# Performance work log

Hardware: AMD Instinct MI355X
Metric: run time of the kernel (lower is better)

## Reference

```python
import jax, jax.numpy as jnp
import numpy as np

K = 3          # conv kernel size
G = 3          # KAN grid intervals
SPLINE_K = 3   # B-spline order
N_BASIS = G + SPLINE_K  # 6


def extended_grid():
    # pykan-style grid on [-1, 1] with G intervals, extended by k knots each side
    h = 2.0 / G
    return jnp.arange(-SPLINE_K, G + SPLINE_K + 1, dtype=jnp.float32) * h - 1.0  # [G+2k+1]


def bspline_basis(x, t, k):
    """Cox-de Boor recursion. x: [...], t: [m] knots -> [..., m-1-k] bases."""
    x = x[..., None]
    b = ((x >= t[:-1]) & (x < t[1:])).astype(x.dtype)  # degree 0: [..., m-1]
    for d in range(1, k + 1):
        left = (x - t[: -(d + 1)]) / (t[d:-1] - t[: -(d + 1)]) * b[..., :-1]
        right = (t[d + 1:] - x) / (t[d + 1:] - t[1:-d]) * b[..., 1:]
        b = left + right
    return b  # [..., m-1-k]


def setup_inputs() -> dict:
    key = jax.random.key(0)
    k1, k2, k3, k4 = jax.random.split(key, 4)
    B, C, H, W = 32, 16, 64, 64
    in_dim, out_dim = C * K * K, 64
    x = jax.random.normal(k1, (B, C, H, W), dtype=jnp.float32)
    coef = jax.random.normal(k2, (in_dim, out_dim, N_BASIS), dtype=jnp.float32) * 0.1
    scale_base = jax.random.normal(k3, (in_dim, out_dim), dtype=jnp.float32) * (1.0 / np.sqrt(in_dim))
    scale_sp = jnp.ones((in_dim, out_dim), dtype=jnp.float32) + 0.0 * jax.random.normal(k4, (in_dim, out_dim))
    return {"x": x, "coef": coef, "scale_base": scale_base, "scale_sp": scale_sp}


def reference(x, coef, scale_base, scale_sp):
    B, C, H, W = x.shape
    Ho, Wo = H - K + 1, W - K + 1
    # im2col with torch-reshape ordering: feature index = c*K*K + di*K + dj
    cols = [x[:, :, di:di + Ho, dj:dj + Wo] for di in range(K) for dj in range(K)]
    patches = jnp.stack(cols, axis=2)                    # [B, C, K*K, Ho, Wo]
    patches = patches.reshape(B, C * K * K, Ho, Wo)      # [B, D, Ho, Wo]
    p = patches.transpose(0, 2, 3, 1)                    # [B, Ho, Wo, D]

    t = extended_grid()
    basis = bspline_basis(p, t, SPLINE_K)                # [B, Ho, Wo, D, N_BASIS]
    # spline part: sum over input dims and bases, with per-edge scale_sp folded into coef
    spline = jnp.einsum('bhwdn,don->bhwo', basis, coef * scale_sp[:, :, None])
    base = jnp.einsum('bhwd,do->bhwo', jax.nn.silu(p), scale_base)
    y = base + spline                                    # [B, Ho, Wo, O]
    return y.transpose(0, 3, 1, 2)                       # [B, O, Ho, Wo]
```

## Files before the change

kernel.cpp:

```cpp
#include <hip/hip_runtime.h>
#include <math.h>

#define Bsz 32
#define Cc  16
#define Hh  64
#define Ww  64
#define HO  62
#define WO  62
#define OD  64
#define ND  144
#define NCHUNK 36
#define BSKEW 520
#define BSM_U16 77824

using short8 = __attribute__((ext_vector_type(8))) short;
using f32x4  = __attribute__((ext_vector_type(4))) float;

__device__ __forceinline__ unsigned short f2bf(float f) {
    union { float f; unsigned u; } v; v.f = f;
    unsigned r = v.u + 0x7fff + ((v.u >> 16) & 1);
    return (unsigned short)(r >> 16);
}
__device__ __forceinline__ float bf2f(unsigned short h) {
    union { unsigned u; float f; } v; v.u = ((unsigned)h) << 16; return v.f;
}

__device__ __forceinline__ uint4 feat_pack(float xv) {
    float xi = (xv + 3.0f) * 1.5f;
    float fi = floorf(xi);
    int   ii = (int)fi;
    float u  = xi - fi;
    float u2 = u * u, u3 = u2 * u;
    float P0 = u3 * (1.0f / 6.0f);
    float P1 = (1.0f + 3.0f * u + 3.0f * u2 - 3.0f * u3) * (1.0f / 6.0f);
    float P2 = (4.0f - 6.0f * u2 + 3.0f * u3) * (1.0f / 6.0f);
    float om = 1.0f - u;
    float P3 = om * om * om * (1.0f / 6.0f);
    bool ok = (ii >= 0) && (ii <= 8);
    float bas[6];
    #pragma unroll
    for (int n = 0; n < 6; ++n) {
        int t = ii - n;
        float v = (t == 0) ? P0 : (t == 1) ? P1 : (t == 2) ? P2 : (t == 3) ? P3 : 0.0f;
        bas[n] = ok ? v : 0.0f;
    }
    float s = xv / (1.0f + __expf(-xv));
    unsigned short sh = f2bf(s);
    unsigned short sl = f2bf(s - bf2f(sh));
    uint4 pk;
    pk.x = (unsigned)f2bf(bas[0]) | ((unsigned)f2bf(bas[1]) << 16);
    pk.y = (unsigned)f2bf(bas[2]) | ((unsigned)f2bf(bas[3]) << 16);
    pk.z = (unsigned)f2bf(bas[4]) | ((unsigned)f2bf(bas[5]) << 16);
    pk.w = (unsigned)sh | ((unsigned)sl << 16);
    return pk;
}

__global__ __launch_bounds__(256) void kan_feat(const float* __restrict__ x,
                                                uint4* __restrict__ fg) {
    int base = blockIdx.x * 2048 + threadIdx.x;
    #pragma unroll
    for (int j = 0; j < 8; ++j) {
        int i = base + j * 256;
        fg[i] = feat_pack(x[i]);
    }
}

__global__ __launch_bounds__(256) void kan_prep2(const float* __restrict__ coef,
                                                 const float* __restrict__ sbase,
                                                 const float* __restrict__ ssp,
                                                 unsigned short* __restrict__ wps) {
    int p = blockIdx.x * 256 + threadIdx.x;
    if (p >= BSM_U16) return;
    int dd  = p / BSKEW;
    int rem = p - dd * BSKEW;
    int o = rem >> 3, n = rem & 7;
    float v = 0.0f;
    if (dd < ND && rem < 512)
        v = (n < 6) ? coef[(dd * OD + o) * 6 + n] * ssp[dd * OD + o] : sbase[dd * OD + o];
    wps[p] = f2bf(v);
}

__global__ __launch_bounds__(512) void kan_gemm(const uint4* __restrict__ fg,
                                                const unsigned short* __restrict__ wps,
                                                float* __restrict__ out) {
    __shared__ unsigned short bsm[BSM_U16];

    const int tid  = threadIdx.x;
    const int bb   = blockIdx.x >> 3;
    const int h    = (blockIdx.x & 7) * 8 + (tid >> 6);
    const int wid  = tid >> 6;
    const int lane = tid & 63;
    const int l15  = lane & 15;
    const int ks   = lane >> 4;
    const bool alive = (h < HO);

    {
        const uint4* src = (const uint4*)wps;
        uint4* dst = (uint4*)bsm;
        #pragma unroll
        for (int it = 0; it < 19; ++it) dst[it * 512 + tid] = src[it * 512 + tid];
    }
    __syncthreads();

    f32x4 acc[4][4];
    #pragma unroll
    for (int rt = 0; rt < 4; ++rt)
        #pragma unroll
        for (int ct = 0; ct < 4; ++ct) acc[rt][ct] = (f32x4){0.f, 0.f, 0.f, 0.f};

    if (alive) {
        const unsigned short* bbase = bsm + ks * BSKEW + l15 * 8;

        auto loadA = [&](int cb, short8* A) {
            int dd  = cb * 4 + ks;
            int c   = (dd * 57) >> 9;
            int rem = dd - c * 9;
            int di  = (rem * 11) >> 5;
            int dj  = rem - di * 3;
            const short8* ap = (const short8*)fg + ((((bb * Cc + c) << 6) + h + di) << 6) + l15 + dj;
            A[0] = ap[0]; A[1] = ap[16]; A[2] = ap[32]; A[3] = ap[48];
        };
        auto loadB = [&](int cb, short8* Bf) {
            const short8* bp = (const short8*)(bbase + cb * 4 * BSKEW);
            Bf[0] = bp[0]; Bf[1] = bp[16]; Bf[2] = bp[32]; Bf[3] = bp[48];
        };

        short8 A0[4], B0[4], A1[4], B1[4];
        loadA(0, A0); loadB(0, B0);
        for (int cb = 0; cb < NCHUNK; cb += 2) {
            loadA(cb + 1, A1); loadB(cb + 1, B1);
            #pragma unroll
            for (int rt = 0; rt < 4; ++rt)
                #pragma unroll
                for (int ct = 0; ct < 4; ++ct)
                    acc[rt][ct] = __builtin_amdgcn_mfma_f32_16x16x32_bf16(A0[rt], B0[ct], acc[rt][ct], 0, 0, 0);
            if (cb + 2 < NCHUNK) { loadA(cb + 2, A0); loadB(cb + 2, B0); }
            #pragma unroll
            for (int rt = 0; rt < 4; ++rt)
                #pragma unroll
                for (int ct = 0; ct < 4; ++ct)
                    acc[rt][ct] = __builtin_amdgcn_mfma_f32_16x16x32_bf16(A1[rt], B1[ct], acc[rt][ct], 0, 0, 0);
        }
    }

    __syncthreads();
    if (alive) {
        float* sc = (float*)bsm + wid * (OD * 68);
        #pragma unroll
        for (int rt = 0; rt < 4; ++rt)
            #pragma unroll
            for (int ct = 0; ct < 4; ++ct)
                *(f32x4*)&sc[(ct * 16 + l15) * 68 + rt * 16 + ks * 4] = acc[rt][ct];
        #pragma unroll 4
        for (int j = 0; j < OD; ++j) {
            float v = sc[j * 68 + lane];
            if (lane < WO) out[((bb * OD + j) * HO + h) * WO + lane] = v;
        }
    }
}

#define FW 68
__global__ __launch_bounds__(256) void kan_prep(const float* __restrict__ coef,
                                                const float* __restrict__ sbase,
                                                const float* __restrict__ ssp,
                                                unsigned short* __restrict__ wp) {
    int idx = blockIdx.x * 256 + threadIdx.x;
    if (idx >= ND * OD * 8) return;
    int n = idx & 7, o = (idx >> 3) & 63, d = idx >> 9;
    float v = (n < 6) ? coef[(d * OD + o) * 6 + n] * ssp[d * OD + o] : sbase[d * OD + o];
    wp[idx] = f2bf(v);
}

__global__ __launch_bounds__(128) void kan_mfma(const float* __restrict__ x,
                                                const unsigned short* __restrict__ wp,
                                                float* __restrict__ out) {
    __shared__ uint4 feat[Cc * 4 * FW];
    const int rp = blockIdx.x, b = blockIdx.y, tid = threadIdx.x;
    const int wid = tid >> 6, lane = tid & 63, l15 = lane & 15, ks = lane >> 4;
    const int hrow0 = rp * 2;
    for (int i = tid; i < Cc * 4 * FW; i += 128) {
        int wl = i % FW, cr = i / FW, r = cr & 3, c = cr >> 2;
        int col = wl < Ww ? wl : Ww - 1;
        feat[i] = feat_pack(x[((b * Cc + c) * Hh + hrow0 + r) * Ww + col]);
    }
    __syncthreads();
    f32x4 acc[4][4];
    #pragma unroll
    for (int rt = 0; rt < 4; ++rt)
        #pragma unroll
        for (int ct = 0; ct < 4; ++ct) acc[rt][ct] = (f32x4){0.f, 0.f, 0.f, 0.f};
    auto loadA = [&](int chunk, short8* A) {
        int d = chunk * 4 + ks;
        int c = (d * 57) >> 9;
        int rem = d - c * 9;
        int di = (rem * 11) >> 5;
        int dj = rem - di * 3;
        const short8* ap = (const short8*)&feat[(c * 4 + wid + di) * FW + l15 + dj];
        A[0] = ap[0]; A[1] = ap[16]; A[2] = ap[32]; A[3] = ap[48];
    };
    auto loadB = [&](int chunk, short8* Bf) {
        int d = chunk * 4 + ks;
        const short8* bp = (const short8*)wp + (d * 64 + l15);
        Bf[0] = bp[0]; Bf[1] = bp[16]; Bf[2] = bp[32]; Bf[3] = bp[48];
    };
    short8 A0[4], B0[4], A1[4], B1[4];
    loadA(0, A0); loadB(0, B0);
    for (int cb = 0; cb < NCHUNK; cb += 2) {
        loadA(cb + 1, A1); loadB(cb + 1, B1);
        #pragma unroll
        for (int rt = 0; rt < 4; ++rt)
            #pragma unroll
            for (int ct = 0; ct < 4; ++ct)
                acc[rt][ct] = __builtin_amdgcn_mfma_f32_16x16x32_bf16(A0[rt], B0[ct], acc[rt][ct], 0, 0, 0);
        if (cb + 2 < NCHUNK) { loadA(cb + 2, A0); loadB(cb + 2, B0); }
        #pragma unroll
        for (int rt = 0; rt < 4; ++rt)
            #pragma unroll
            for (int ct = 0; ct < 4; ++ct)
                acc[rt][ct] = __builtin_amdgcn_mfma_f32_16x16x32_bf16(A1[rt], B1[ct], acc[rt][ct], 0, 0, 0);
    }
    __syncthreads();
    float* sC = ((float*)feat) + wid * (OD * FW);
    #pragma unroll
    for (int rt = 0; rt < 4; ++rt)
        #pragma unroll
        for (int ct = 0; ct < 4; ++ct)
            *(f32x4*)&sC[(ct * 16 + l15) * FW + rt * 16 + ks * 4] = acc[rt][ct];
    const int orow = hrow0 + wid;
    for (int j = 0; j < OD; ++j) {
        float v = sC[j * FW + lane];
        if (lane < WO) out[((b * OD + j) * HO + orow) * WO + lane] = v;
    }
}

extern "C" void kernel_launch(void* const* d_in, const int* in_sizes, int n_in,
                              void* d_out, int out_size, void* d_ws, size_t ws_size,
                              hipStream_t stream) {
    (void)in_sizes; (void)n_in; (void)out_size;
    const float* x     = (const float*)d_in[0];
    const float* coef  = (const float*)d_in[1];
    const float* sbase = (const float*)d_in[2];
    const float* ssp   = (const float*)d_in[3];
    float* out = (float*)d_out;

    const size_t wps_bytes  = (size_t)BSM_U16 * 2;
    const size_t featg_bytes = (size_t)Bsz * Cc * Hh * Ww * 16;
    const size_t need = wps_bytes + featg_bytes + 64;

    if (ws_size >= need) {
        unsigned short* wps = (unsigned short*)d_ws;
        uint4* fg = (uint4*)((char*)d_ws + wps_bytes);
        kan_feat<<<1024, 256, 0, stream>>>(x, fg);
        kan_prep2<<<(BSM_U16 + 255) / 256, 256, 0, stream>>>(coef, sbase, ssp, wps);
        kan_gemm<<<256, 512, 0, stream>>>(fg, wps, out);
    } else if (ws_size >= (size_t)ND * OD * 8 * 2) {
        unsigned short* wp = (unsigned short*)d_ws;
        kan_prep<<<(ND * OD * 8 + 255) / 256, 256, 0, stream>>>(coef, sbase, ssp, wp);
        dim3 grid(HO / 2, Bsz);
        kan_mfma<<<grid, 128, 0, stream>>>(x, wp, out);
    }
}
```

Before: 48.29 us.

## Restructure KAN GEMM with 32x32 MFMA, LDS double-buffered async loads

Replaces the previous GEMM kernel with one where each 256-thread block computes two output rows for one batch. It stages both the feature tile and a K-chunk of weights into double-buffered LDS using global_load_lds, then runs 32x32x16 bf16 MFMAs. The weights are no longer kept whole in LDS, which cuts LDS use and allows more blocks per CU. The grid becomes 31x32 blocks instead of 256. The silu pair is packed so the duplicated base weight multiplies the hi and lo silu parts. The cost is a __syncthreads per K-chunk and smaller per-block reuse.

```diff
diff --git a/kernel.cpp b/kernel.cpp
--- a/kernel.cpp
+++ b/kernel.cpp
@@ -9,20 +9,27 @@
 #define WO  62
 #define OD  64
 #define ND  144
-#define NCHUNK 36
-#define BSKEW 520
-#define BSM_U16 77824
+#define KC  18
 
 using short8 = __attribute__((ext_vector_type(8))) short;
 using f32x4  = __attribute__((ext_vector_type(4))) float;
-
-__device__ __forceinline__ unsigned short f2bf(float f) {
+using f32x16 = __attribute__((ext_vector_type(16))) float;
+typedef unsigned int u32;
+typedef unsigned short ushort;
+
+__device__ __forceinline__ ushort f2bf(float f) {
     union { float f; unsigned u; } v; v.f = f;
     unsigned r = v.u + 0x7fff + ((v.u >> 16) & 1);
-    return (unsigned short)(r >> 16);
-}
-__device__ __forceinline__ float bf2f(unsigned short h) {
+    return (ushort)(r >> 16);
+}
+__device__ __forceinline__ float bf2f(ushort h) {
     union { unsigned u; float f; } v; v.u = ((unsigned)h) << 16; return v.f;
+}
+
+__device__ __forceinline__ void gload_lds16(const void* g, void* l) {
+    __builtin_amdgcn_global_load_lds((const __attribute__((address_space(1))) u32*)g,
+                                     (__attribute__((address_space(3))) u32*)l,
+                                     16, 0, 0);
 }
 
 __device__ __forceinline__ uint4 feat_pack(float xv) {
@@ -45,8 +52,8 @@
         bas[n] = ok ? v : 0.0f;
     }
     float s = xv / (1.0f + __expf(-xv));
-    unsigned short sh = f2bf(s);
-    unsigned short sl = f2bf(s - bf2f(sh));
+    ushort sh = f2bf(s);
+    ushort sl = f2bf(s - bf2f(sh));
     uint4 pk;
     pk.x = (unsigned)f2bf(bas[0]) | ((unsigned)f2bf(bas[1]) << 16);
     pk.y = (unsigned)f2bf(bas[2]) | ((unsigned)f2bf(bas[3]) << 16);
@@ -65,105 +72,121 @@
     }
 }
 
-__global__ __launch_bounds__(256) void kan_prep2(const float* __restrict__ coef,
+__global__ __launch_bounds__(256) void kan_prep3(const float* __restrict__ coef,
                                                  const float* __restrict__ sbase,
                                                  const float* __restrict__ ssp,
-                                                 unsigned short* __restrict__ wps) {
-    int p = blockIdx.x * 256 + threadIdx.x;
-    if (p >= BSM_U16) return;
-    int dd  = p / BSKEW;
-    int rem = p - dd * BSKEW;
-    int o = rem >> 3, n = rem & 7;
-    float v = 0.0f;
-    if (dd < ND && rem < 512)
-        v = (n < 6) ? coef[(dd * OD + o) * 6 + n] * ssp[dd * OD + o] : sbase[dd * OD + o];
-    wps[p] = f2bf(v);
-}
-
-__global__ __launch_bounds__(512) void kan_gemm(const uint4* __restrict__ fg,
-                                                const unsigned short* __restrict__ wps,
-                                                float* __restrict__ out) {
-    __shared__ unsigned short bsm[BSM_U16];
+                                                 ushort* __restrict__ wpb) {
+    int g = blockIdx.x * 256 + threadIdx.x;
+    if (g >= KC * 8 * 64) return;
+    int n = g & 63, d = g >> 6;
+    float sspv = ssp[d * OD + n];
+    ushort sb = f2bf(sbase[d * OD + n]);
+    ushort v[8];
+    #pragma unroll
+    for (int f = 0; f < 6; ++f) v[f] = f2bf(coef[(d * OD + n) * 6 + f] * sspv);
+    v[6] = sb; v[7] = sb;
+    uint4 pk;
+    pk.x = (unsigned)v[0] | ((unsigned)v[1] << 16);
+    pk.y = (unsigned)v[2] | ((unsigned)v[3] << 16);
+    pk.z = (unsigned)v[4] | ((unsigned)v[5] << 16);
+    pk.w = (unsigned)v[6] | ((unsigned)v[7] << 16);
+    *(uint4*)&wpb[(size_t)g * 8] = pk;
+}
+
+__global__ __launch_bounds__(256, 3) void kan_gemm2(const uint4* __restrict__ fg,
+                                                    const uint4* __restrict__ wpb,
+                                                    float* __restrict__ out) {
+    __shared__ uint4 ldsmem[3072];
+    char* lds = (char*)ldsmem;
 
     const int tid  = threadIdx.x;
-    const int bb   = blockIdx.x >> 3;
-    const int h    = (blockIdx.x & 7) * 8 + (tid >> 6);
     const int wid  = tid >> 6;
     const int lane = tid & 63;
-    const int l15  = lane & 15;
-    const int ks   = lane >> 4;
-    const bool alive = (h < HO);
-
-    {
-        const uint4* src = (const uint4*)wps;
-        uint4* dst = (uint4*)bsm;
-        #pragma unroll
-        for (int it = 0; it < 19; ++it) dst[it * 512 + tid] = src[it * 512 + tid];
-    }
-    __syncthreads();
-
-    f32x4 acc[4][4];
-    #pragma unroll
-    for (int rt = 0; rt < 4; ++rt)
-        #pragma unroll
-        for (int ct = 0; ct < 4; ++ct) acc[rt][ct] = (f32x4){0.f, 0.f, 0.f, 0.f};
-
-    if (alive) {
-        const unsigned short* bbase = bsm + ks * BSKEW + l15 * 8;
-
-        auto loadA = [&](int cb, short8* A) {
-            int dd  = cb * 4 + ks;
-            int c   = (dd * 57) >> 9;
-            int rem = dd - c * 9;
+    const int l31  = lane & 31;
+    const int hi   = lane >> 5;
+    const int mt   = blockIdx.x;
+    const int bb   = blockIdx.y;
+    const int h0   = mt * 2;
+
+    auto stage = [&](int kc, int bufsel) {
+        char* bufA = lds + bufsel * 24576;
+        char* bufB = bufA + 16384;
+        #pragma unroll
+        for (int q = 0; q < 2; ++q) {
+            int s = wid + q * 4;
+            int d = kc * 8 + s;
+            int c   = (d * 57) >> 9;
+            int rem = d - c * 9;
             int di  = (rem * 11) >> 5;
             int dj  = rem - di * 3;
-            const short8* ap = (const short8*)fg + ((((bb * Cc + c) << 6) + h + di) << 6) + l15 + dj;
-            A[0] = ap[0]; A[1] = ap[16]; A[2] = ap[32]; A[3] = ap[48];
-        };
-        auto loadB = [&](int cb, short8* Bf) {
-            const short8* bp = (const short8*)(bbase + cb * 4 * BSKEW);
-            Bf[0] = bp[0]; Bf[1] = bp[16]; Bf[2] = bp[32]; Bf[3] = bp[48];
-        };
-
-        short8 A0[4], B0[4], A1[4], B1[4];
-        loadA(0, A0); loadB(0, B0);
-        for (int cb = 0; cb < NCHUNK; cb += 2) {
-            loadA(cb + 1, A1); loadB(cb + 1, B1);
+            int su  = c * 4096 + (h0 + di) * 64 + dj;
             #pragma unroll
-            for (int rt = 0; rt < 4; ++rt)
-                #pragma unroll
-                for (int ct = 0; ct < 4; ++ct)
-                    acc[rt][ct] = __builtin_amdgcn_mfma_f32_16x16x32_bf16(A0[rt], B0[ct], acc[rt][ct], 0, 0, 0);
-            if (cb + 2 < NCHUNK) { loadA(cb + 2, A0); loadB(cb + 2, B0); }
-            #pragma unroll
-            for (int rt = 0; rt < 4; ++rt)
-                #pragma unroll
-                for (int ct = 0; ct < 4; ++ct)
-                    acc[rt][ct] = __builtin_amdgcn_mfma_f32_16x16x32_bf16(A1[rt], B1[ct], acc[rt][ct], 0, 0, 0);
-        }
-    }
-
-    __syncthreads();
-    if (alive) {
-        float* sc = (float*)bsm + wid * (OD * 68);
-        #pragma unroll
-        for (int rt = 0; rt < 4; ++rt)
-            #pragma unroll
-            for (int ct = 0; ct < 4; ++ct)
-                *(f32x4*)&sc[(ct * 16 + l15) * 68 + rt * 16 + ks * 4] = acc[rt][ct];
-        #pragma unroll 4
-        for (int j = 0; j < OD; ++j) {
-            float v = sc[j * 68 + lane];
-            if (lane < WO) out[((bb * OD + j) * HO + h) * WO + lane] = v;
-        }
-    }
-}
-
+            for (int hh = 0; hh < 2; ++hh) {
+                const char* src = (const char*)fg +
+                    ((size_t)(bb * 65536 + su + hh * 64 + lane) * 16);
+                gload_lds16(src, bufA + (s * 128 + hh * 64) * 16);
+            }
+        }
+        #pragma unroll
+        for (int q = 0; q < 2; ++q) {
+            int kb = wid + q * 4;
+            const char* src = (const char*)wpb + ((size_t)(kc * 512 + kb * 64 + lane) * 16);
+            gload_lds16(src, bufB + kb * 1024);
+        }
+    };
+
+    f32x16 acc0, acc1;
+    #pragma unroll
+    for (int i = 0; i < 16; ++i) { acc0[i] = 0.0f; acc1[i] = 0.0f; }
+
+    stage(0, 0);
+    __syncthreads();
+
+    const int m0 = wid * 32 + l31;
+
+    #pragma unroll
+    for (int kc = 0; kc < KC; ++kc) {
+        const int cur = kc & 1;
+        if (kc + 1 < KC) stage(kc + 1, cur ^ 1);
+        const ushort* A  = (const ushort*)(lds + cur * 24576);
+        const ushort* Bw = (const ushort*)(lds + cur * 24576 + 16384);
+        #pragma unroll
+        for (int kk = 0; kk < 4; ++kk) {
+            const int sl = kk * 2 + hi;
+            short8 a  = *(const short8*)(A  + (size_t)(sl * 128 + m0) * 8);
+            short8 b0 = *(const short8*)(Bw + (size_t)(sl * 64 + l31) * 8);
+            short8 b1 = *(const short8*)(Bw + (size_t)(sl * 64 + 32 + l31) * 8);
+            acc0 = __builtin_amdgcn_mfma_f32_32x32x16_bf16(a, b0, acc0, 0, 0, 0);
+            acc1 = __builtin_amdgcn_mfma_f32_32x32x16_bf16(a, b1, acc1, 0, 0, 0);
+        }
+        __syncthreads();
+    }
+
+    float* Csc = (float*)lds;
+    #pragma unroll
+    for (int r = 0; r < 16; ++r) {
+        int ml = (r & 3) + ((r >> 2) << 3) + (hi << 2);
+        Csc[(size_t)l31 * 130 + wid * 32 + ml]        = acc0[r];
+        Csc[(size_t)(32 + l31) * 130 + wid * 32 + ml] = acc1[r];
+    }
+    __syncthreads();
+    #pragma unroll
+    for (int it = 0; it < 16; ++it) {
+        int flat = it * 256 + tid;
+        int o = flat >> 6, hh = (flat >> 5) & 1, fc = flat & 31;
+        if (fc < 31) {
+            float2 v = *(float2*)&Csc[(size_t)o * 130 + hh * 64 + fc * 2];
+            *(float2*)&out[((size_t)(bb * OD + o) * HO + h0 + hh) * WO + fc * 2] = v;
+        }
+    }
+}
+
+#define NCHUNK 36
 #define FW 68
 __global__ __launch_bounds__(256) void kan_prep(const float* __restrict__ coef,
                                                 const float* __restrict__ sbase,
                                                 const float* __restrict__ ssp,
-                                                unsigned short* __restrict__ wp) {
+                                                ushort* __restrict__ wp) {
     int idx = blockIdx.x * 256 + threadIdx.x;
     if (idx >= ND * OD * 8) return;
     int n = idx & 7, o = (idx >> 3) & 63, d = idx >> 9;
@@ -172,7 +195,7 @@
 }
 
 __global__ __launch_bounds__(128) void kan_mfma(const float* __restrict__ x,
-                                                const unsigned short* __restrict__ wp,
+                                                const ushort* __restrict__ wp,
                                                 float* __restrict__ out) {
     __shared__ uint4 feat[Cc * 4 * FW];
     const int rp = blockIdx.x, b = blockIdx.y, tid = threadIdx.x;
@@ -243,18 +266,19 @@
     const float* ssp   = (const float*)d_in[3];
     float* out = (float*)d_out;
 
-    const size_t wps_bytes  = (size_t)BSM_U16 * 2;
-    const size_t featg_bytes = (size_t)Bsz * Cc * Hh * Ww * 16;
-    const size_t need = wps_bytes + featg_bytes + 64;
+    const size_t wpb_bytes = (size_t)KC * 512 * 16;
+    const size_t fg_bytes  = (size_t)Bsz * Cc * Hh * Ww * 16;
+    const size_t need = wpb_bytes + fg_bytes + 4096;
 
     if (ws_size >= need) {
-        unsigned short* wps = (unsigned short*)d_ws;
-        uint4* fg = (uint4*)((char*)d_ws + wps_bytes);
+        uint4* wpb = (uint4*)d_ws;
+        uint4* fg  = (uint4*)((char*)d_ws + wpb_bytes);
         kan_feat<<<1024, 256, 0, stream>>>(x, fg);
-        kan_prep2<<<(BSM_U16 + 255) / 256, 256, 0, stream>>>(coef, sbase, ssp, wps);
-        kan_gemm<<<256, 512, 0, stream>>>(fg, wps, out);
+        kan_prep3<<<36, 256, 0, stream>>>(coef, sbase, ssp, (ushort*)wpb);
+        dim3 grid(31, Bsz);
+        kan_gemm2<<<grid, 256, 0, stream>>>(fg, wpb, out);
     } else if (ws_size >= (size_t)ND * OD * 8 * 2) {
-        unsigned short* wp = (unsigned short*)d_ws;
+        ushort* wp = (ushort*)d_ws;
         kan_prep<<<(ND * OD * 8 + 255) / 256, 256, 0, stream>>>(coef, sbase, ssp, wp);
         dim3 grid(HO / 2, Bsz);
         kan_mfma<<<grid, 128, 0, stream>>>(x, wp, out);
```

Measured after the change: 51.99 us. 7.7% more time.
